# Performance work log

Hardware: AMD Instinct MI355X
Metric: run time of the kernel (lower is better)

The kernel has to match this reference:

```python
import jax, jax.numpy as jnp
import numpy as np
from jax import lax

N, CIN, COUT, K = 16, 3, 16, 3
D = H = W = 64

def setup_inputs() -> dict:
    key = jax.random.key(0)
    k1, k2, k3 = jax.random.split(key, 3)
    x = jax.random.normal(k1, (N, CIN, D, H, W), dtype=jnp.float32)
    # torch Conv3d default init scale ~ 1/sqrt(fan_in); plain normals are fine for a baseline
    fan_in = CIN * K * K * K
    weight = jax.random.normal(k2, (COUT, CIN, K, K, K), dtype=jnp.float32) / np.sqrt(fan_in)
    bias = jax.random.normal(k3, (COUT,), dtype=jnp.float32) * 0.01
    return {"x": x, "weight": weight, "bias": bias}

def reference(x, weight, bias):
    # Conv3d, stride 1, no padding (NCDHW / OIDHW)
    y = lax.conv_general_dilated(
        x, weight,
        window_strides=(1, 1, 1),
        padding="VALID",
        dimension_numbers=("NCDHW", "OIDHW", "NCDHW"),
    )
    y = y + bias[None, :, None, None, None]          # [N, C, D', H', W']
    m = jnp.min(y, axis=2)                            # min over D -> [N, C, H', W']
    return jax.nn.softmax(m, axis=1)                  # softmax over channels
```

## Files before the change

### kernel.cpp

```cpp
#include <hip/hip_runtime.h>
#include <math.h>


#define CH 4

__global__ __launch_bounds__(1024)
void conv3d_min_softmax(
    const float* __restrict__ x,
    const float* __restrict__ wgt,
    const float* __restrict__ bias,
    float* __restrict__ out)
{
    const int tid = threadIdx.x;
    const int wv   = __builtin_amdgcn_readfirstlane(tid >> 6);
    const int half = wv & 1;
    const int co0  = (wv >> 1) * 2;
    const int co1  = co0 + 1;
    const int l    = tid & 63;
    const int r0   = half * 4 + (l >> 4);
    const int cg   = l & 15;
    const int wc   = cg * 2;
    const int n    = blockIdx.z;
    const int h0   = blockIdx.y * 8;
    const int w0   = blockIdx.x * 32;

    __shared__ __align__(16) float sx[2][4320];
    __shared__ float sm[256 * 17];

    int goff[2];
#pragma unroll
    for (int k = 0; k < 2; ++k) {
        int F = tid + 1024 * k;
        if (F > 1079) F = 1079;
        int ci  = F / 360;
        int rem = F - ci * 360;
        int dd  = rem / 90;
        int rr  = rem - dd * 90;
        int rw  = rr / 9;
        int g   = rr - rw * 9;
        int gh  = h0 + rw;  if (gh > 63) gh = 63;
        int gw  = w0 + g * 4; if (gw > 60) gw = 60;
        goff[k] = (((ci * 64 + dd) * 64 + gh) * 64 + gw) * 4;
    }
    const char* xb = (const char*)(x + (size_t)n * 3 * 64 * 64 * 64);

    float A0acc[6][2], A1acc[6][2];
#pragma unroll
    for (int j = 0; j < 6; ++j)
#pragma unroll
        for (int p = 0; p < 2; ++p) { A0acc[j][p] = 0.f; A1acc[j][p] = 0.f; }
    float mv0[2] = {1e30f, 1e30f};
    float mv1[2] = {1e30f, 1e30f};

    {
        char* lb = (char*)&sx[0][0];
        __builtin_amdgcn_global_load_lds(
            (const void*)(xb + goff[0]), (void*)(lb + tid * 16), 16, 0, 0);
        if (tid < 56)
            __builtin_amdgcn_global_load_lds(
                (const void*)(xb + goff[1]),
                (void*)(lb + (1024 + tid) * 16), 16, 0, 0);
    }

    for (int c = 0; c < 16; ++c) {
        __syncthreads();

        if (c < 15) {
            const char* xc = xb + (size_t)(c + 1) * (CH * 64 * 64 * 4);
            char* lb = (char*)&sx[(c + 1) & 1][0];
            __builtin_amdgcn_global_load_lds(
                (const void*)(xc + goff[0]), (void*)(lb + tid * 16),
                16, 0, 0);
            if (tid < 56)
                __builtin_amdgcn_global_load_lds(
                    (const void*)(xc + goff[1]),
                    (void*)(lb + (1024 + tid) * 16), 16, 0, 0);
        }

        const float* S = sx[c & 1];

#pragma unroll 1
        for (int ci = 0; ci < 3; ++ci) {
            float ws0[27], ws1[27];
            {
                const float* wp0 = wgt + (co0 * 3 + ci) * 27;
                const float* wp1 = wgt + (co1 * 3 + ci) * 27;
#pragma unroll
                for (int i = 0; i < 27; ++i) { ws0[i] = wp0[i]; ws1[i] = wp1[i]; }
            }
            const float* Sci = S + ci * (CH * 10 * 36) + r0 * 36 + wc;
#pragma unroll
            for (int dd = 0; dd < CH; ++dd) {
#pragma unroll
                for (int kh = 0; kh < 3; ++kh) {
                    const float2 a = *(const float2*)&Sci[(dd * 10 + kh) * 36];
                    const float2 b =
                        *(const float2*)&Sci[(dd * 10 + kh) * 36 + 2];
                    const float row[4] = {a.x, a.y, b.x, b.y};
#pragma unroll
                    for (int kw = 0; kw < 3; ++kw) {
                        const float w00 = ws0[0  + kh * 3 + kw];
                        const float w01 = ws0[9  + kh * 3 + kw];
                        const float w02 = ws0[18 + kh * 3 + kw];
                        const float w10 = ws1[0  + kh * 3 + kw];
                        const float w11 = ws1[9  + kh * 3 + kw];
                        const float w12 = ws1[18 + kh * 3 + kw];
#pragma unroll
                        for (int p = 0; p < 2; ++p) {
                            const float xv = row[kw + p];
                            A0acc[dd + 2][p] = fmaf(xv, w00, A0acc[dd + 2][p]);
                            A0acc[dd + 1][p] = fmaf(xv, w01, A0acc[dd + 1][p]);
                            A0acc[dd + 0][p] = fmaf(xv, w02, A0acc[dd + 0][p]);
                            A1acc[dd + 2][p] = fmaf(xv, w10, A1acc[dd + 2][p]);
                            A1acc[dd + 1][p] = fmaf(xv, w11, A1acc[dd + 1][p]);
                            A1acc[dd + 0][p] = fmaf(xv, w12, A1acc[dd + 0][p]);
                        }
                    }
                }
            }
        }

        const bool full = (c > 0);
#pragma unroll
        for (int j = 0; j < 4; ++j) {
            if (j >= 2 || full) {
#pragma unroll
                for (int p = 0; p < 2; ++p) {
                    mv0[p] = fminf(mv0[p], A0acc[j][p]);
                    mv1[p] = fminf(mv1[p], A1acc[j][p]);
                }
            }
        }
#pragma unroll
        for (int p = 0; p < 2; ++p) {
            A0acc[0][p] = A0acc[4][p]; A0acc[1][p] = A0acc[5][p];
            A1acc[0][p] = A1acc[4][p]; A1acc[1][p] = A1acc[5][p];
        }
#pragma unroll
        for (int j = 2; j < 6; ++j)
#pragma unroll
            for (int p = 0; p < 2; ++p) { A0acc[j][p] = 0.f; A1acc[j][p] = 0.f; }
    }

    const float bv0 = bias[co0];
    const float bv1 = bias[co1];
    const int px0 = r0 * 32 + wc;
#pragma unroll
    for (int pp = 0; pp < 2; ++pp) {
        sm[(px0 + pp) * 17 + co0] = mv0[pp] + bv0;
        sm[(px0 + pp) * 17 + co1] = mv1[pp] + bv1;
    }
    __syncthreads();

    const int hp = h0 + r0;
#pragma unroll
    for (int pp = 0; pp < 2; ++pp) {
        const int px = px0 + pp;
        float mx = -1e30f;
#pragma unroll
        for (int j = 0; j < 16; ++j) mx = fmaxf(mx, sm[px * 17 + j]);
        float sum = 0.f;
#pragma unroll
        for (int j = 0; j < 16; ++j) sum += __expf(sm[px * 17 + j] - mx);
        const int wp = w0 + wc + pp;
        if (hp < 62 && wp < 62) {
            const float e0 = __expf(sm[px * 17 + co0] - mx);
            const float e1 = __expf(sm[px * 17 + co1] - mx);
            out[(((size_t)n * 16 + co0) * 62 + hp) * 62 + wp] = e0 / sum;
            out[(((size_t)n * 16 + co1) * 62 + hp) * 62 + wp] = e1 / sum;
        }
    }
}

extern "C" void kernel_launch(void* const* d_in, const int* in_sizes, int n_in,
                              void* d_out, int out_size, void* d_ws, size_t ws_size,
                              hipStream_t stream) {
    const float* x    = (const float*)d_in[0];
    const float* wgt  = (const float*)d_in[1];
    const float* bias = (const float*)d_in[2];
    float* out        = (float*)d_out;
    dim3 grid(2, 8, 16);
    dim3 block(1024);
    hipLaunchKernelGGL(conv3d_min_softmax, grid, block, 0, stream,
                       x, wgt, bias, out);
}
```

Before: 198.8 us.

## Split depth reduction across two blocks with atomic min and separate softmax pass

```diff
diff --git a/kernel.cpp b/kernel.cpp
--- a/kernel.cpp
+++ b/kernel.cpp
@@ -4,12 +4,20 @@
 
 #define CH 4
 
+__device__ __forceinline__ unsigned enc_min(float f) {
+    unsigned u = __float_as_uint(f);
+    return (u & 0x80000000u) ? ~u : (u | 0x80000000u);
+}
+__device__ __forceinline__ float dec_min(unsigned k) {
+    unsigned u = (k & 0x80000000u) ? (k ^ 0x80000000u) : ~k;
+    return __uint_as_float(u);
+}
+
 __global__ __launch_bounds__(1024)
-void conv3d_min_softmax(
+void conv3d_min_part(
     const float* __restrict__ x,
     const float* __restrict__ wgt,
-    const float* __restrict__ bias,
-    float* __restrict__ out)
+    unsigned* __restrict__ outk)
 {
     const int tid = threadIdx.x;
     const int wv   = __builtin_amdgcn_readfirstlane(tid >> 6);
@@ -20,12 +28,16 @@
     const int r0   = half * 4 + (l >> 4);
     const int cg   = l & 15;
     const int wc   = cg * 2;
-    const int n    = blockIdx.z;
+    const int z    = blockIdx.z;
+    const int n    = z >> 1;
+    const int dh   = z & 1;
+    const int base = dh * 28;
+    const int lo   = dh * 30;
+    const int hi   = lo + 31;
     const int h0   = blockIdx.y * 8;
     const int w0   = blockIdx.x * 32;
 
     __shared__ __align__(16) float sx[2][4320];
-    __shared__ float sm[256 * 17];
 
     int goff[2];
 #pragma unroll
@@ -40,7 +52,7 @@
         int g   = rr - rw * 9;
         int gh  = h0 + rw;  if (gh > 63) gh = 63;
         int gw  = w0 + g * 4; if (gw > 60) gw = 60;
-        goff[k] = (((ci * 64 + dd) * 64 + gh) * 64 + gw) * 4;
+        goff[k] = (((ci * 64 + base + dd) * 64 + gh) * 64 + gw) * 4;
     }
     const char* xb = (const char*)(x + (size_t)n * 3 * 64 * 64 * 64);
 
@@ -62,10 +74,10 @@
                 (void*)(lb + (1024 + tid) * 16), 16, 0, 0);
     }
 
-    for (int c = 0; c < 16; ++c) {
+    for (int c = 0; c < 9; ++c) {
         __syncthreads();
 
-        if (c < 15) {
+        if (c < 8) {
             const char* xc = xb + (size_t)(c + 1) * (CH * 64 * 64 * 4);
             char* lb = (char*)&sx[(c + 1) & 1][0];
             __builtin_amdgcn_global_load_lds(
@@ -120,10 +132,10 @@
             }
         }
 
-        const bool full = (c > 0);
+        const int dpb = base + c * 4 - 2;
 #pragma unroll
         for (int j = 0; j < 4; ++j) {
-            if (j >= 2 || full) {
+            if (dpb + j >= lo && dpb + j <= hi) {
 #pragma unroll
                 for (int p = 0; p < 2; ++p) {
                     mv0[p] = fminf(mv0[p], A0acc[j][p]);
@@ -142,34 +154,46 @@
             for (int p = 0; p < 2; ++p) { A0acc[j][p] = 0.f; A1acc[j][p] = 0.f; }
     }
 
-    const float bv0 = bias[co0];
-    const float bv1 = bias[co1];
-    const int px0 = r0 * 32 + wc;
+    const int hp = h0 + r0;
 #pragma unroll
     for (int pp = 0; pp < 2; ++pp) {
-        sm[(px0 + pp) * 17 + co0] = mv0[pp] + bv0;
-        sm[(px0 + pp) * 17 + co1] = mv1[pp] + bv1;
-    }
-    __syncthreads();
-
-    const int hp = h0 + r0;
-#pragma unroll
-    for (int pp = 0; pp < 2; ++pp) {
-        const int px = px0 + pp;
-        float mx = -1e30f;
-#pragma unroll
-        for (int j = 0; j < 16; ++j) mx = fmaxf(mx, sm[px * 17 + j]);
-        float sum = 0.f;
-#pragma unroll
-        for (int j = 0; j < 16; ++j) sum += __expf(sm[px * 17 + j] - mx);
         const int wp = w0 + wc + pp;
         if (hp < 62 && wp < 62) {
-            const float e0 = __expf(sm[px * 17 + co0] - mx);
-            const float e1 = __expf(sm[px * 17 + co1] - mx);
-            out[(((size_t)n * 16 + co0) * 62 + hp) * 62 + wp] = e0 / sum;
-            out[(((size_t)n * 16 + co1) * 62 + hp) * 62 + wp] = e1 / sum;
-        }
-    }
+            atomicMin(&outk[(((size_t)n * 16 + co0) * 62 + hp) * 62 + wp],
+                      enc_min(mv0[pp]));
+            atomicMin(&outk[(((size_t)n * 16 + co1) * 62 + hp) * 62 + wp],
+                      enc_min(mv1[pp]));
+        }
+    }
+}
+
+__global__ __launch_bounds__(256)
+void softmax_fin(
+    unsigned* __restrict__ outk,
+    const float* __restrict__ bias)
+{
+    const int tid = threadIdx.x;
+    const int c   = tid & 15;
+    const int pxi = blockIdx.x * 16 + (tid >> 4);
+    const int n   = pxi / 3844;
+    const int rem = pxi - n * 3844;
+    const int hp  = rem / 62;
+    const int wp  = rem - hp * 62;
+
+    const size_t idx = (((size_t)n * 16 + c) * 62 + hp) * 62 + wp;
+    float v = dec_min(outk[idx]) + bias[c];
+
+    float mx = v;
+#pragma unroll
+    for (int off = 1; off < 16; off <<= 1)
+        mx = fmaxf(mx, __shfl_xor(mx, off, 64));
+    float e = __expf(v - mx);
+    float sum = e;
+#pragma unroll
+    for (int off = 1; off < 16; off <<= 1)
+        sum += __shfl_xor(sum, off, 64);
+
+    ((float*)outk)[idx] = e / sum;
 }
 
 extern "C" void kernel_launch(void* const* d_in, const int* in_sizes, int n_in,
@@ -178,9 +202,14 @@
     const float* x    = (const float*)d_in[0];
     const float* wgt  = (const float*)d_in[1];
     const float* bias = (const float*)d_in[2];
-    float* out        = (float*)d_out;
-    dim3 grid(2, 8, 16);
-    dim3 block(1024);
-    hipLaunchKernelGGL(conv3d_min_softmax, grid, block, 0, stream,
-                       x, wgt, bias, out);
-}
+
+    hipMemsetAsync(d_out, 0xFF, (size_t)out_size * sizeof(float), stream);
+
+    dim3 g1(2, 8, 32);
+    hipLaunchKernelGGL(conv3d_min_part, g1, dim3(1024), 0, stream,
+                       x, wgt, (unsigned*)d_out);
+
+    dim3 g2(3844);
+    hipLaunchKernelGGL(softmax_fin, g2, dim3(256), 0, stream,
+                       (unsigned*)d_out, bias);
+}
```

After: 224.7 us. 1.13x slower.
